# Performance work log

Hardware: AMD Instinct MI355X
Metric: run time of the kernel (lower is better)

The kernel has to match this reference:

```python
import jax, jax.numpy as jnp
import numpy as np


def sign_ste(x):
    # forward: sign(x); backward: grad * (|x| <= 1)  (straight-through estimator)
    # clip has exactly the STE gradient mask; stop_gradient swaps in sign(x) for fwd value.
    c = jnp.clip(x, -1.0, 1.0)
    return c + jax.lax.stop_gradient(jnp.sign(x) - c)


def setup_inputs() -> dict:
    key = jax.random.key(0)
    k1, k2, k3 = jax.random.split(key, 3)
    N, CIN, COUT = 8192, 4096, 4096
    input_x = jax.random.normal(k1, (N, CIN), dtype=jnp.float32)
    weight = jax.random.normal(k2, (COUT, CIN), dtype=jnp.float32) * 0.02
    bias = jax.random.normal(k3, (COUT,), dtype=jnp.float32) * 0.01
    return {"input_x": input_x, "weight": weight, "bias": bias}


def reference(input_x, weight, bias):
    qw = sign_ste(weight)            # [COUT, CIN], values in {-1, 0, +1}
    qx = sign_ste(input_x)           # [N, CIN]
    out = jnp.einsum('nc,oc->no', qx, qw)  # binary GEMM executed as float matmul
    alpha = jnp.mean(jnp.abs(weight))
    betta = jnp.mean(jnp.abs(input_x))
    return out * alpha * betta + bias
```

## Files before the change

kernel.cpp:

```cpp
#include <hip/hip_runtime.h>
#include <stdint.h>

#define N_ROWS 8192
#define C_IN   4096
#define C_OUT  4096
#define NCHUNK (C_IN / 64)
#define MT4    65536

typedef int   v4i  __attribute__((ext_vector_type(4)));
typedef int   v8i  __attribute__((ext_vector_type(8)));
typedef float v16f __attribute__((ext_vector_type(16)));

__global__ void pack_all_kernel(const float* __restrict__ x,
                                const float* __restrict__ w,
                                uint8_t* __restrict__ xf,
                                uint8_t* __restrict__ wf,
                                float* __restrict__ partials) {
    __shared__ __align__(16) uint16_t tile16[4096];
    __shared__ float sacc[4];

    const int b = blockIdx.x;
    const float* src; uint8_t* dst; int slab;
    if (b < 2048) { src = x; dst = xf; slab = b; }
    else          { src = w; dst = wf; slab = b - 2048; }
    const int mt = slab >> 3, cg = slab & 7;

    const int t = threadIdx.x;
    const int r = t >> 3, lc = t & 7;

    const float4* base = (const float4*)(src + (size_t)(mt * 32 + r) * C_IN + cg * 512) + lc;
    float acc = 0.f;
#pragma unroll
    for (int it = 0; it < 16; ++it) {
        float4 v = base[it * 8];
        uint16_t nv = (uint16_t)((v.x > 0.f ? 0x2u : 0xAu)
                               | (v.y > 0.f ? 0x2u : 0xAu) << 4
                               | (v.z > 0.f ? 0x2u : 0xAu) << 8
                               | (v.w > 0.f ? 0x2u : 0xAu) << 12);
        acc += fabsf(v.x) + fabsf(v.y) + fabsf(v.z) + fabsf(v.w);
        tile16[it * 256 + t] = nv;
    }
    __syncthreads();
    uint4* gout = (uint4*)(dst + (size_t)mt * MT4 + (size_t)cg * 8192);
    const uint4* lin = (const uint4*)tile16;
#pragma unroll
    for (int p = 0; p < 2; ++p) gout[p * 256 + t] = lin[p * 256 + t];

    for (int off = 32; off > 0; off >>= 1) acc += __shfl_down(acc, off, 64);
    const int lane = t & 63, wv = t >> 6;
    if (lane == 0) sacc[wv] = acc;
    __syncthreads();
    if (t == 0) {
        float s = 0.f;
        for (int i = 0; i < 4; ++i) s += sacc[i];
        partials[b] = s;
    }
}

__global__ void finalize_kernel(const float* __restrict__ part_x, int nx,
                                const float* __restrict__ part_w, int nw,
                                float* __restrict__ out_ab) {
    __shared__ float s[256];
    float ax = 0.f;
    for (int i = threadIdx.x; i < nx; i += 256) ax += part_x[i];
    s[threadIdx.x] = ax; __syncthreads();
    for (int st = 128; st > 0; st >>= 1) {
        if (threadIdx.x < st) s[threadIdx.x] += s[threadIdx.x + st];
        __syncthreads();
    }
    float sumx = s[0];
    __syncthreads();
    float aw = 0.f;
    for (int i = threadIdx.x; i < nw; i += 256) aw += part_w[i];
    s[threadIdx.x] = aw; __syncthreads();
    for (int st = 128; st > 0; st >>= 1) {
        if (threadIdx.x < st) s[threadIdx.x] += s[threadIdx.x + st];
        __syncthreads();
    }
    if (threadIdx.x == 0) {
        float sumw = s[0];
        float alpha = sumw / (float)((long long)C_OUT * C_IN);
        float betta = sumx / (float)((long long)N_ROWS * C_IN);
        out_ab[0] = alpha * betta;
    }
}

#define MF(a, b, c) \
    __builtin_amdgcn_mfma_scale_f32_32x32x64_f8f6f4( \
        __builtin_shufflevector((a), (a), 0, 1, 2, 3, -1, -1, -1, -1), \
        __builtin_shufflevector((b), (b), 0, 1, 2, 3, -1, -1, -1, -1), \
        (c), 4, 4, 0, 127, 0, 127)

__launch_bounds__(512, 2)
__global__ void xnor_gemm_fp4(const uint8_t* __restrict__ Afrag,
                              const uint8_t* __restrict__ Bfrag,
                              const float* __restrict__ bias,
                              const float* __restrict__ ab_ptr,
                              float* __restrict__ out) {
    const int t    = threadIdx.x;
    const int lane = t & 63;
    const int hi   = lane >> 5;
    const int r    = lane & 31;
    const int wid  = t >> 6;
    const int wr   = wid >> 2;
    const int wc   = wid & 3;

    const int id  = blockIdx.x;
    const int swz = (id & 7) * 64 + (id >> 3);
    const int brow = (swz >> 4) * 256;
    const int bcol = (swz & 15) * 256;

    const uint8_t* pa[4];
    const uint8_t* pb[2];
#pragma unroll
    for (int m = 0; m < 4; ++m)
        pa[m] = Afrag + (size_t)((brow >> 5) + wr * 4 + m) * MT4 + (size_t)lane * 16;
#pragma unroll
    for (int n = 0; n < 2; ++n)
        pb[n] = Bfrag + (size_t)((bcol >> 5) + wc * 2 + n) * MT4 + (size_t)lane * 16;

#define LOADSET(AS, BS, c)                                                  \
    do {                                                                    \
        AS[0] = *(const v4i*)(pa[0] + (size_t)(c) * 1024);                  \
        AS[1] = *(const v4i*)(pa[1] + (size_t)(c) * 1024);                  \
        AS[2] = *(const v4i*)(pa[2] + (size_t)(c) * 1024);                  \
        AS[3] = *(const v4i*)(pa[3] + (size_t)(c) * 1024);                  \
        BS[0] = *(const v4i*)(pb[0] + (size_t)(c) * 1024);                  \
        BS[1] = *(const v4i*)(pb[1] + (size_t)(c) * 1024);                  \
    } while (0)

#define DOMFMA(AS, BS)                                \
    do {                                              \
        __builtin_amdgcn_s_setprio(1);                \
        acc[0][0] = MF(AS[0], BS[0], acc[0][0]);      \
        acc[0][1] = MF(AS[0], BS[1], acc[0][1]);      \
        acc[1][0] = MF(AS[1], BS[0], acc[1][0]);      \
        acc[1][1] = MF(AS[1], BS[1], acc[1][1]);      \
        acc[2][0] = MF(AS[2], BS[0], acc[2][0]);      \
        acc[2][1] = MF(AS[2], BS[1], acc[2][1]);      \
        acc[3][0] = MF(AS[3], BS[0], acc[3][0]);      \
        acc[3][1] = MF(AS[3], BS[1], acc[3][1]);      \
        __builtin_amdgcn_s_setprio(0);                \
    } while (0)

    v16f acc[4][2] = {};
    v4i A0[4], B0[2], A1[4], B1[2];

    LOADSET(A0, B0, 0);

    for (int cb = 0; cb < NCHUNK; cb += 2) {
        LOADSET(A1, B1, cb + 1);
        DOMFMA(A0, B0);
        if (cb + 2 < NCHUNK) LOADSET(A0, B0, cb + 2);
        DOMFMA(A1, B1);
    }

    const float ab = ab_ptr[0];
#pragma unroll
    for (int m = 0; m < 4; ++m) {
#pragma unroll
        for (int n = 0; n < 2; ++n) {
            int col = bcol + wc * 64 + n * 32 + r;
            float bv = bias[col];
#pragma unroll
            for (int reg = 0; reg < 16; ++reg) {
                int rowf = (reg & 3) + 8 * (reg >> 2) + 4 * hi;
                int grow = brow + wr * 128 + m * 32 + rowf;
                out[(size_t)grow * C_OUT + col] = acc[m][n][reg] * ab + bv;
            }
        }
    }
#undef LOADSET
#undef DOMFMA
}

extern "C" void kernel_launch(void* const* d_in, const int* in_sizes, int n_in,
                              void* d_out, int out_size, void* d_ws, size_t ws_size,
                              hipStream_t stream) {
    const float* x    = (const float*)d_in[0];
    const float* w    = (const float*)d_in[1];
    const float* bias = (const float*)d_in[2];
    float* out = (float*)d_out;

    char* ws = (char*)d_ws;
    float* red      = (float*)ws;
    float* partials = red + 16;
    uint8_t* xs  = (uint8_t*)(ws + 16384);
    uint8_t* wsg = xs + (size_t)N_ROWS * C_IN / 2;

    pack_all_kernel<<<3072, 256, 0, stream>>>(x, w, xs, wsg, partials);
    finalize_kernel<<<1, 256, 0, stream>>>(partials, 2048, partials + 2048, 1024, red);

    dim3 grid((N_ROWS / 256) * (C_OUT / 256));
    xnor_gemm_fp4<<<grid, 512, 0, stream>>>(xs, wsg, bias, red, out);
}
```

Measured before the change: 147.3 us.

## Stage A fragments through LDS with direct global-to-LDS loads, 4-deep ring

Replaces the per-wave direct global loads of A fragments with block-shared staging: each thread issues a global_load_lds of 16 bytes into a 4-slot LDS ring, and waves then read their A fragments from LDS. This removes redundant global traffic, since the two column-waves of each row group previously fetched the same A data separately. B stays in registers with direct loads. The change adds explicit vmcnt waits and a barrier per chunk, which may stall the MFMA pipeline, and relies on hand-tuned counter values being correct.

```diff
diff --git a/kernel.cpp b/kernel.cpp
--- a/kernel.cpp
+++ b/kernel.cpp
@@ -8,7 +8,6 @@
 #define MT4    65536
 
 typedef int   v4i  __attribute__((ext_vector_type(4)));
-typedef int   v8i  __attribute__((ext_vector_type(8)));
 typedef float v16f __attribute__((ext_vector_type(16)));
 
 __global__ void pack_all_kernel(const float* __restrict__ x,
@@ -97,6 +96,8 @@
                               const float* __restrict__ bias,
                               const float* __restrict__ ab_ptr,
                               float* __restrict__ out) {
+    __shared__ __align__(16) uint8_t lds[4][8192];
+
     const int t    = threadIdx.x;
     const int lane = t & 63;
     const int hi   = lane >> 5;
@@ -110,23 +111,29 @@
     const int brow = (swz >> 4) * 256;
     const int bcol = (swz & 15) * 256;
 
-    const uint8_t* pa[4];
-    const uint8_t* pb[2];
-#pragma unroll
-    for (int m = 0; m < 4; ++m)
-        pa[m] = Afrag + (size_t)((brow >> 5) + wr * 4 + m) * MT4 + (size_t)lane * 16;
-#pragma unroll
-    for (int n = 0; n < 2; ++n)
-        pb[n] = Bfrag + (size_t)((bcol >> 5) + wc * 2 + n) * MT4 + (size_t)lane * 16;
-
-#define LOADSET(AS, BS, c)                                                  \
-    do {                                                                    \
-        AS[0] = *(const v4i*)(pa[0] + (size_t)(c) * 1024);                  \
-        AS[1] = *(const v4i*)(pa[1] + (size_t)(c) * 1024);                  \
-        AS[2] = *(const v4i*)(pa[2] + (size_t)(c) * 1024);                  \
-        AS[3] = *(const v4i*)(pa[3] + (size_t)(c) * 1024);                  \
-        BS[0] = *(const v4i*)(pb[0] + (size_t)(c) * 1024);                  \
-        BS[1] = *(const v4i*)(pb[1] + (size_t)(c) * 1024);                  \
+    const uint8_t* Abase = Afrag + (size_t)(brow >> 5) * MT4;
+    const size_t soff = (size_t)(t >> 6) * MT4 + (size_t)(t & 63) * 16;
+
+    const uint8_t* pb0 = Bfrag + (size_t)((bcol >> 5) + wc * 2 + 0) * MT4 + (size_t)lane * 16;
+    const uint8_t* pb1 = Bfrag + (size_t)((bcol >> 5) + wc * 2 + 1) * MT4 + (size_t)lane * 16;
+
+#define STG_A(BUF, c)                                                                   \
+    __builtin_amdgcn_global_load_lds(                                                   \
+        (const __attribute__((address_space(1))) void*)(Abase + soff + (size_t)(c) * 1024), \
+        (__attribute__((address_space(3))) void*)(&lds[BUF][t * 16]), 16, 0, 0)
+
+#define LOADB(BS, c)                                              \
+    do {                                                          \
+        BS[0] = *(const v4i*)(pb0 + (size_t)(c) * 1024);          \
+        BS[1] = *(const v4i*)(pb1 + (size_t)(c) * 1024);          \
+    } while (0)
+
+#define LOADA(AS, BUF)                                                           \
+    do {                                                                         \
+        AS[0] = *(const v4i*)(&lds[BUF][((wr * 4 + 0) * 64 + lane) * 16]);       \
+        AS[1] = *(const v4i*)(&lds[BUF][((wr * 4 + 1) * 64 + lane) * 16]);       \
+        AS[2] = *(const v4i*)(&lds[BUF][((wr * 4 + 2) * 64 + lane) * 16]);       \
+        AS[3] = *(const v4i*)(&lds[BUF][((wr * 4 + 3) * 64 + lane) * 16]);       \
     } while (0)
 
 #define DOMFMA(AS, BS)                                \
@@ -143,16 +150,38 @@
         __builtin_amdgcn_s_setprio(0);                \
     } while (0)
 
+#define BODY(cexp, CA, CB, NA, NB, NBUF, SBUF)                                      \
+    do {                                                                            \
+        const int c_ = (cexp);                                                      \
+        if (c_ + 1 < NCHUNK) LOADB(NB, c_ + 1);                                     \
+        if (c_ + 2 < NCHUNK) {                                                      \
+            STG_A(SBUF, c_ + 2);                                                    \
+            asm volatile("s_waitcnt vmcnt(3)" ::: "memory");                        \
+        } else if (c_ + 1 < NCHUNK) {                                               \
+            asm volatile("s_waitcnt vmcnt(2)" ::: "memory");                        \
+        } else {                                                                    \
+            asm volatile("s_waitcnt vmcnt(0)" ::: "memory");                        \
+        }                                                                           \
+        __builtin_amdgcn_s_barrier();                                               \
+        if (c_ + 1 < NCHUNK) LOADA(NA, NBUF);                                       \
+        DOMFMA(CA, CB);                                                             \
+    } while (0)
+
     v16f acc[4][2] = {};
     v4i A0[4], B0[2], A1[4], B1[2];
 
-    LOADSET(A0, B0, 0);
-
-    for (int cb = 0; cb < NCHUNK; cb += 2) {
-        LOADSET(A1, B1, cb + 1);
-        DOMFMA(A0, B0);
-        if (cb + 2 < NCHUNK) LOADSET(A0, B0, cb + 2);
-        DOMFMA(A1, B1);
+    STG_A(0, 0);
+    LOADB(B0, 0);
+    STG_A(1, 1);
+    asm volatile("s_waitcnt vmcnt(3)" ::: "memory");
+    __builtin_amdgcn_s_barrier();
+    LOADA(A0, 0);
+
+    for (int cb = 0; cb < NCHUNK; cb += 4) {
+        BODY(cb + 0, A0, B0, A1, B1, 1, 2);
+        BODY(cb + 1, A1, B1, A0, B0, 2, 3);
+        BODY(cb + 2, A0, B0, A1, B1, 3, 0);
+        BODY(cb + 3, A1, B1, A0, B0, 0, 1);
     }
 
     const float ab = ab_ptr[0];
@@ -170,8 +199,11 @@
             }
         }
     }
-#undef LOADSET
+#undef STG_A
+#undef LOADB
+#undef LOADA
 #undef DOMFMA
+#undef BODY
 }
 
 extern "C" void kernel_launch(void* const* d_in, const int* in_sizes, int n_in,
```

Result: faster. 143.7 us (-2.4%).

## Stage GEMM operand fragments through LDS to share loads across waves

Applied to the files above, without the earlier changes.

Each wave used to load its own A and B fragments straight from global memory, so waves in the same row or column fetched the same data again. Now all 512 threads load each chunk of the block's 256x256 tile once, write it into a 4-buffer LDS ring, and each wave reads its fragments from LDS after a barrier. This cuts global and L2 traffic per block but adds a block-wide barrier every chunk, LDS writes and reads, and 64KB of LDS per block, which may limit occupancy to the intended 2 blocks per CU.

```diff
diff --git a/kernel.cpp b/kernel.cpp
--- a/kernel.cpp
+++ b/kernel.cpp
@@ -8,7 +8,6 @@
 #define MT4    65536
 
 typedef int   v4i  __attribute__((ext_vector_type(4)));
-typedef int   v8i  __attribute__((ext_vector_type(8)));
 typedef float v16f __attribute__((ext_vector_type(16)));
 
 __global__ void pack_all_kernel(const float* __restrict__ x,
@@ -97,6 +96,8 @@
                               const float* __restrict__ bias,
                               const float* __restrict__ ab_ptr,
                               float* __restrict__ out) {
+    __shared__ __align__(16) uint8_t lds[4][16384];
+
     const int t    = threadIdx.x;
     const int lane = t & 63;
     const int hi   = lane >> 5;
@@ -110,23 +111,30 @@
     const int brow = (swz >> 4) * 256;
     const int bcol = (swz & 15) * 256;
 
-    const uint8_t* pa[4];
-    const uint8_t* pb[2];
-#pragma unroll
-    for (int m = 0; m < 4; ++m)
-        pa[m] = Afrag + (size_t)((brow >> 5) + wr * 4 + m) * MT4 + (size_t)lane * 16;
-#pragma unroll
-    for (int n = 0; n < 2; ++n)
-        pb[n] = Bfrag + (size_t)((bcol >> 5) + wc * 2 + n) * MT4 + (size_t)lane * 16;
-
-#define LOADSET(AS, BS, c)                                                  \
+    const uint8_t* Abase = Afrag + (size_t)(brow >> 5) * MT4;
+    const uint8_t* Bbase = Bfrag + (size_t)(bcol >> 5) * MT4;
+    const size_t soff = (size_t)(t >> 6) * MT4 + (size_t)(t & 63) * 16;
+
+#define GLOAD(GA, GB, c)                                                    \
     do {                                                                    \
-        AS[0] = *(const v4i*)(pa[0] + (size_t)(c) * 1024);                  \
-        AS[1] = *(const v4i*)(pa[1] + (size_t)(c) * 1024);                  \
-        AS[2] = *(const v4i*)(pa[2] + (size_t)(c) * 1024);                  \
-        AS[3] = *(const v4i*)(pa[3] + (size_t)(c) * 1024);                  \
-        BS[0] = *(const v4i*)(pb[0] + (size_t)(c) * 1024);                  \
-        BS[1] = *(const v4i*)(pb[1] + (size_t)(c) * 1024);                  \
+        GA = *(const uint4*)(Abase + soff + (size_t)(c) * 1024);            \
+        GB = *(const uint4*)(Bbase + soff + (size_t)(c) * 1024);            \
+    } while (0)
+
+#define SWRITE(GA, GB, BUF)                                                 \
+    do {                                                                    \
+        *(uint4*)(&lds[BUF][t * 16])        = GA;                           \
+        *(uint4*)(&lds[BUF][8192 + t * 16]) = GB;                           \
+    } while (0)
+
+#define LOADFRAGS(AS, BS, BUF)                                                        \
+    do {                                                                              \
+        AS[0] = *(const v4i*)(&lds[BUF][((wr * 4 + 0) * 64 + lane) * 16]);            \
+        AS[1] = *(const v4i*)(&lds[BUF][((wr * 4 + 1) * 64 + lane) * 16]);            \
+        AS[2] = *(const v4i*)(&lds[BUF][((wr * 4 + 2) * 64 + lane) * 16]);            \
+        AS[3] = *(const v4i*)(&lds[BUF][((wr * 4 + 3) * 64 + lane) * 16]);            \
+        BS[0] = *(const v4i*)(&lds[BUF][8192 + ((wc * 2 + 0) * 64 + lane) * 16]);     \
+        BS[1] = *(const v4i*)(&lds[BUF][8192 + ((wc * 2 + 1) * 64 + lane) * 16]);     \
     } while (0)
 
 #define DOMFMA(AS, BS)                                \
@@ -143,16 +151,31 @@
         __builtin_amdgcn_s_setprio(0);                \
     } while (0)
 
+#define BODY(cexp, CA, CB, NA, NB, WGA, WGB, LGA, LGB)                              \
+    do {                                                                            \
+        const int c_ = (cexp);                                                      \
+        if (c_ + 2 < NCHUNK) GLOAD(LGA, LGB, c_ + 2);                               \
+        if (c_ + 1 < NCHUNK) SWRITE(WGA, WGB, (c_ + 1) & 3);                        \
+        asm volatile("s_waitcnt lgkmcnt(0)" ::: "memory");                          \
+        __builtin_amdgcn_s_barrier();                                               \
+        if (c_ + 1 < NCHUNK) LOADFRAGS(NA, NB, (c_ + 1) & 3);                       \
+        DOMFMA(CA, CB);                                                             \
+    } while (0)
+
     v16f acc[4][2] = {};
     v4i A0[4], B0[2], A1[4], B1[2];
-
-    LOADSET(A0, B0, 0);
+    uint4 GaA, GaB, GbA, GbB;
+
+    GLOAD(GbA, GbB, 0);
+    GLOAD(GaA, GaB, 1);
+    SWRITE(GbA, GbB, 0);
+    asm volatile("s_waitcnt lgkmcnt(0)" ::: "memory");
+    __builtin_amdgcn_s_barrier();
+    LOADFRAGS(A0, B0, 0);
 
     for (int cb = 0; cb < NCHUNK; cb += 2) {
-        LOADSET(A1, B1, cb + 1);
-        DOMFMA(A0, B0);
-        if (cb + 2 < NCHUNK) LOADSET(A0, B0, cb + 2);
-        DOMFMA(A1, B1);
+        BODY(cb + 0, A0, B0, A1, B1, GaA, GaB, GbA, GbB);
+        BODY(cb + 1, A1, B1, A0, B0, GbA, GbB, GaA, GaB);
     }
 
     const float ab = ab_ptr[0];
@@ -170,8 +193,11 @@
             }
         }
     }
-#undef LOADSET
+#undef GLOAD
+#undef SWRITE
+#undef LOADFRAGS
 #undef DOMFMA
+#undef BODY
 }
 
 extern "C" void kernel_launch(void* const* d_in, const int* in_sizes, int n_in,
```

Result: slower. 157.4 us (+6.9%).
